# Kernel optimization log

Measured on AMD Instinct MI355X. Metric: run time of the kernel, lower is better.

## Reference

```python
import jax, jax.numpy as jnp
import numpy as np

N = 50000   # num entities
R = 230     # num relations (doubled for inverses -> 460)
H = 128     # hidden dim
T = 8       # timesteps (sequence_len)
E = 600000  # edges per timestep graph
L = 2       # num RGCN layers
RRELU_SLOPE = (1.0 / 8.0 + 1.0 / 3.0) / 2.0  # F.rrelu eval-mode slope


def _l2norm(x):
    # F.normalize: L2 over last dim, eps=1e-12
    return x / jnp.maximum(jnp.linalg.norm(x, axis=-1, keepdims=True), 1e-12)


def setup_inputs() -> dict:
    key = jax.random.key(0)
    ks = jax.random.split(key, 10)
    src = jax.random.randint(ks[0], (T, E), 0, N)
    dst = jax.random.randint(ks[1], (T, E), 0, N)
    etype = jax.random.randint(ks[2], (T, E), 0, 2 * R)
    emb_ent = jax.random.normal(ks[3], (N, H), jnp.float32)
    emb_rel = jax.random.normal(ks[4], (2 * R, H), jnp.float32) * 0.05
    w_neigh = jax.random.normal(ks[5], (L, H, H), jnp.float32) * 0.05
    w_loop = jax.random.normal(ks[6], (L, H, H), jnp.float32) * 0.05
    w_evolve = jax.random.normal(ks[7], (L, H, H), jnp.float32) * 0.05
    tg_w = jax.random.normal(ks[8], (H, H), jnp.float32) * 0.05
    tg_b = jnp.zeros((H,), jnp.float32)
    return {"emb_ent": emb_ent, "emb_rel": emb_rel, "w_neigh": w_neigh,
            "w_loop": w_loop, "w_evolve": w_evolve, "tg_w": tg_w,
            "tg_b": tg_b, "src": src, "dst": dst, "etype": etype}


def reference(emb_ent, emb_rel, w_neigh, w_loop, w_evolve, tg_w, tg_b, src, dst, etype):
    # rgcn receives emb_rel.data (detached) in the torch module
    rel = jax.lax.stop_gradient(emb_rel)

    def rgcn(h, s, d, t):
        indeg = jax.ops.segment_sum(jnp.ones(s.shape, h.dtype), d, num_segments=N)
        norm = 1.0 / jnp.maximum(indeg, 1.0)          # g.ndata['norm']
        has_in = (indeg > 0)[:, None]
        for l in range(L):
            msg = (h[s] + rel[t]) @ w_neigh[l]          # [E,H]
            agg = jax.ops.segment_sum(msg, d, num_segments=N) * norm[:, None]
            loop = jnp.where(has_in, h @ w_loop[l], h @ w_evolve[l])
            z = agg + loop
            h = jnp.where(z >= 0, z, RRELU_SLOPE * z)   # rrelu (eval mode)
        return h

    def step(h, edges):
        s, d, t = edges
        cur = _l2norm(rgcn(h, s, d, t))                 # layer_norm=True
        tw = jax.nn.sigmoid(h @ tg_w + tg_b)            # time gate
        h_new = tw * cur + (1.0 - tw) * h
        return h_new, h_new

    h0 = _l2norm(emb_ent)
    _, hist = jax.lax.scan(step, h0, (src, dst, etype))
    history_embs = jnp.concatenate([h0[None], hist], axis=0)  # [T+1,N,H]
    return history_embs, emb_rel
```

## Files before the change

### kernel.cpp

```cpp
#include <hip/hip_runtime.h>

#define N_ENT 50000
#define H 128
#define NREL 460
#define T_STEPS 8
#define NEDGE 600000
#define SLOPE 0.22916666666666666f
#define NBUK 391
#define EPB 4096
#define ZCAP 8192

typedef __attribute__((ext_vector_type(8))) short bf16x8;
typedef __attribute__((ext_vector_type(8))) unsigned short us8;
typedef __attribute__((ext_vector_type(4))) float f32x4;
typedef unsigned short u16;
typedef unsigned int u32;
typedef unsigned long long u64;

__device__ __forceinline__ float b2f(u16 u) {
  union { u32 i; float f; } v; v.i = ((u32)u) << 16; return v.f;
}
__device__ __forceinline__ u16 f2b(float f) {
  union { float f; u32 i; } v; v.f = f;
  return (u16)((v.i + 0x7FFFu + ((v.i >> 16) & 1u)) >> 16);
}
__device__ __forceinline__ float wave_sum(float v) {
#pragma unroll
  for (int off = 32; off > 0; off >>= 1) v += __shfl_xor(v, off, 64);
  return v;
}

__global__ void convw_kernel(const float* __restrict__ wn, const float* __restrict__ wl,
                             const float* __restrict__ tg, u16* __restrict__ wbt) {
  int m = blockIdx.x >> 6;
  int f = ((blockIdx.x & 63) << 8) + threadIdx.x;
  int n = f >> 7, k = f & 127;
  const float* src;
  switch (m) {
    case 0: src = wn; break;
    case 1: src = wl; break;
    case 2: src = wn + 16384; break;
    case 3: src = wl + 16384; break;
    default: src = tg; break;
  }
  wbt[m * 16384 + n * 128 + k] = f2b(src[k * 128 + n]);
}

__global__ void convrel_kernel(const float* __restrict__ rel, u16* __restrict__ relb) {
  int i = blockIdx.x * 256 + threadIdx.x;
  relb[i] = f2b(rel[i]);
}

__global__ void l2norm_kernel(const float* __restrict__ in, float* __restrict__ out,
                              u16* __restrict__ outb) {
  int row = blockIdx.x * 4 + (threadIdx.x >> 6);
  int lane = threadIdx.x & 63;
  size_t base = (size_t)row * H;
  float2 v = ((const float2*)(in + base))[lane];
  float ss = wave_sum(v.x * v.x + v.y * v.y);
  float inv = 1.0f / fmaxf(sqrtf(ss), 1e-12f);
  float2 o = {v.x * inv, v.y * inv};
  ((float2*)(out + base))[lane] = o;
  ushort2 ob; ob.x = f2b(o.x); ob.y = f2b(o.y);
  ((ushort2*)(outb + base))[lane] = ob;
}

__global__ __launch_bounds__(256) void bucket_count(const int* __restrict__ dst,
                                                    int* __restrict__ bcnt) {
  int t = blockIdx.y;
  __shared__ int lc[NBUK];
  for (int j = threadIdx.x; j < NBUK; j += 256) lc[j] = 0;
  __syncthreads();
  for (int i = blockIdx.x * 256 + threadIdx.x; i < NEDGE; i += 64 * 256)
    atomicAdd(&lc[dst[(size_t)t * NEDGE + i] >> 7], 1);
  __syncthreads();
  for (int j = threadIdx.x; j < NBUK; j += 256)
    if (lc[j]) atomicAdd(&bcnt[t * NBUK + j], lc[j]);
}

__global__ __launch_bounds__(512) void bucket_scan(const int* __restrict__ bcnt,
                                                   int* __restrict__ bstart,
                                                   int* __restrict__ curA,
                                                   int* __restrict__ zcnt) {
  int t = blockIdx.x, tid = threadIdx.x;
  if (tid == 0) zcnt[t] = 0;
  __shared__ int s[512];
  int v = (tid < NBUK) ? bcnt[t * NBUK + tid] : 0;
  s[tid] = v;
  __syncthreads();
  for (int off = 1; off < 512; off <<= 1) {
    int u = (tid >= off) ? s[tid - off] : 0;
    __syncthreads();
    s[tid] += u;
    __syncthreads();
  }
  if (tid < NBUK) {
    int ex = s[tid] - v;
    bstart[t * NBUK + tid] = ex;
    curA[t * NBUK + tid] = ex;
  }
}

__global__ __launch_bounds__(256) void passA_kernel(const int* __restrict__ src,
                                                    const int* __restrict__ dst,
                                                    const int* __restrict__ ety,
                                                    int* curA, u64* __restrict__ tmp) {
  int t = blockIdx.y;
  __shared__ int cnt[NBUK], base[NBUK];
  for (int j = threadIdx.x; j < NBUK; j += 256) cnt[j] = 0;
  __syncthreads();
  int e0 = blockIdx.x * EPB;
  int e1 = e0 + EPB < NEDGE ? e0 + EPB : NEDGE;
  for (int i = e0 + threadIdx.x; i < e1; i += 256)
    atomicAdd(&cnt[dst[(size_t)t * NEDGE + i] >> 7], 1);
  __syncthreads();
  for (int j = threadIdx.x; j < NBUK; j += 256) {
    int c = cnt[j];
    base[j] = c ? atomicAdd(&curA[t * NBUK + j], c) : 0;
    cnt[j] = 0;
  }
  __syncthreads();
  for (int i = e0 + threadIdx.x; i < e1; i += 256) {
    size_t o = (size_t)t * NEDGE + i;
    int d = dst[o];
    int j = d >> 7;
    int p = base[j] + atomicAdd(&cnt[j], 1);
    tmp[(size_t)t * NEDGE + p] = ((u64)d << 32) | (u32)src[o] | ((u32)ety[o] << 17);
  }
}

__global__ __launch_bounds__(256) void passB_kernel(const u64* __restrict__ tmp,
                                                    const int* __restrict__ bstart,
                                                    int* __restrict__ rp,
                                                    u32* __restrict__ edges,
                                                    int* __restrict__ zcnt,
                                                    int* __restrict__ zlist) {
  int t = blockIdx.y, b = blockIdx.x, tid = threadIdx.x;
  int start = bstart[t * NBUK + b];
  int end = (b + 1 < NBUK) ? bstart[t * NBUK + b + 1] : NEDGE;
  __shared__ int cnt[128], scn[128], cur[128];
  if (tid < 128) cnt[tid] = 0;
  __syncthreads();
  for (int i = start + tid; i < end; i += 256)
    atomicAdd(&cnt[(int)((tmp[(size_t)t * NEDGE + i] >> 32) & 127)], 1);
  __syncthreads();
  if (tid < 128) scn[tid] = cnt[tid];
  __syncthreads();
  for (int off = 1; off < 128; off <<= 1) {
    int u = (tid < 128 && tid >= off) ? scn[tid - off] : 0;
    __syncthreads();
    if (tid < 128) scn[tid] += u;
    __syncthreads();
  }
  if (tid < 128) {
    int rs = start + scn[tid] - cnt[tid];
    cur[tid] = rs;
    int gd = (b << 7) + tid;
    if (gd < N_ENT) {
      rp[t * N_ENT + gd] = rs + cnt[tid];
      if (cnt[tid] == 0) {
        int p = atomicAdd(&zcnt[t], 1);
        if (p < ZCAP) zlist[t * ZCAP + p] = gd;
      }
    }
  }
  __syncthreads();
  for (int i = start + tid; i < end; i += 256) {
    u64 e = tmp[(size_t)t * NEDGE + i];
    int p = atomicAdd(&cur[(int)((e >> 32) & 127)], 1);
    edges[(size_t)t * NEDGE + p] = (u32)e;
  }
}

__global__ __launch_bounds__(256) void gather_kernel(const u16* __restrict__ hb,
                                                     const u16* __restrict__ relb,
                                                     const int* __restrict__ rp,
                                                     const u32* __restrict__ edges,
                                                     u16* __restrict__ aggb) {
  int d = blockIdx.x * 16 + (threadIdx.x >> 4);
  int q = threadIdx.x & 15;
  int start = d ? rp[d - 1] : 0, end = rp[d];
  float a[8] = {};
  int i = start;
  for (; i + 4 <= end; i += 4) {
    u32 e0 = edges[i], e1 = edges[i + 1], e2 = edges[i + 2], e3 = edges[i + 3];
    us8 h0 = *(const us8*)(hb + (size_t)(e0 & 0x1FFFF) * H + q * 8);
    us8 r0 = *(const us8*)(relb + (size_t)(e0 >> 17) * H + q * 8);
    us8 h1 = *(const us8*)(hb + (size_t)(e1 & 0x1FFFF) * H + q * 8);
    us8 r1 = *(const us8*)(relb + (size_t)(e1 >> 17) * H + q * 8);
    us8 h2 = *(const us8*)(hb + (size_t)(e2 & 0x1FFFF) * H + q * 8);
    us8 r2 = *(const us8*)(relb + (size_t)(e2 >> 17) * H + q * 8);
    us8 h3 = *(const us8*)(hb + (size_t)(e3 & 0x1FFFF) * H + q * 8);
    us8 r3 = *(const us8*)(relb + (size_t)(e3 >> 17) * H + q * 8);
#pragma unroll
    for (int j = 0; j < 8; j++)
      a[j] += (b2f(h0[j]) + b2f(r0[j])) + (b2f(h1[j]) + b2f(r1[j])) +
              (b2f(h2[j]) + b2f(r2[j])) + (b2f(h3[j]) + b2f(r3[j]));
  }
  for (; i < end; i++) {
    u32 e0 = edges[i];
    us8 h0 = *(const us8*)(hb + (size_t)(e0 & 0x1FFFF) * H + q * 8);
    us8 r0 = *(const us8*)(relb + (size_t)(e0 >> 17) * H + q * 8);
#pragma unroll
    for (int j = 0; j < 8; j++) a[j] += b2f(h0[j]) + b2f(r0[j]);
  }
  int deg = end - start;
  float nm = 1.0f / (float)(deg > 0 ? deg : 1);
  us8 o;
#pragma unroll
  for (int j = 0; j < 8; j++) o[j] = f2b(a[j] * nm);
  *(us8*)(aggb + (size_t)d * H + q * 8) = o;
}

__global__ __launch_bounds__(256) void rgcn_gemm0(
    const u16* __restrict__ A1, const u16* __restrict__ A2,
    const u16* __restrict__ B1t, const u16* __restrict__ B2t, u16* __restrict__ Cb) {
  int wave = threadIdx.x >> 6, lane = threadIdx.x & 63;
  int row0 = blockIdx.x * 64 + wave * 16;
  int ar = lane & 15, kg = lane >> 4;
  int arow = row0 + ar;
  if (arow >= N_ENT) arow = N_ENT - 1;
  bf16x8 a1[4], a2[4];
#pragma unroll
  for (int s = 0; s < 4; s++) {
    a1[s] = *(const bf16x8*)(A1 + (size_t)arow * H + s * 32 + kg * 8);
    a2[s] = *(const bf16x8*)(A2 + (size_t)arow * H + s * 32 + kg * 8);
  }
  f32x4 acc[8];
  f32x4 z = {0.f, 0.f, 0.f, 0.f};
#pragma unroll
  for (int n = 0; n < 8; n++) acc[n] = z;
#pragma unroll
  for (int n = 0; n < 8; n++) {
    const u16* b1p = B1t + (size_t)(n * 16 + ar) * H + kg * 8;
    const u16* b2p = B2t + (size_t)(n * 16 + ar) * H + kg * 8;
#pragma unroll
    for (int s = 0; s < 4; s++) {
      bf16x8 b1 = *(const bf16x8*)(b1p + s * 32);
      bf16x8 b2 = *(const bf16x8*)(b2p + s * 32);
      acc[n] = __builtin_amdgcn_mfma_f32_16x16x32_bf16(a1[s], b1, acc[n], 0, 0, 0);
      acc[n] = __builtin_amdgcn_mfma_f32_16x16x32_bf16(a2[s], b2, acc[n], 0, 0, 0);
    }
  }
#pragma unroll
  for (int n = 0; n < 8; n++) {
    int c = ar + n * 16;
#pragma unroll
    for (int r = 0; r < 4; r++) {
      int gr = row0 + kg * 4 + r;
      if (gr < N_ENT) {
        float v = acc[n][r];
        v = v >= 0.f ? v : SLOPE * v;
        Cb[(size_t)gr * H + c] = f2b(v);
      }
    }
  }
}

__global__ __launch_bounds__(256) void step_final(
    const u16* __restrict__ aggb, const u16* __restrict__ hAb, const u16* hbio,
    const u16* __restrict__ B1t, const u16* __restrict__ B2t, const u16* __restrict__ B3t,
    const float* __restrict__ tgb, const float* __restrict__ h_t, float* __restrict__ h_n,
    u16* hb_out) {
  int wave = threadIdx.x >> 6, lane = threadIdx.x & 63;
  int row0 = blockIdx.x * 64 + wave * 16;
  int ar = lane & 15, kg = lane >> 4;
  int arow = row0 + ar;
  if (arow >= N_ENT) arow = N_ENT - 1;
  bf16x8 a1[4], a2[4], a3[4];
#pragma unroll
  for (int s = 0; s < 4; s++) {
    a1[s] = *(const bf16x8*)(aggb + (size_t)arow * H + s * 32 + kg * 8);
    a2[s] = *(const bf16x8*)(hAb + (size_t)arow * H + s * 32 + kg * 8);
    a3[s] = *(const bf16x8*)(hbio + (size_t)arow * H + s * 32 + kg * 8);
  }
  f32x4 accm[8], accg[8];
  f32x4 z4 = {0.f, 0.f, 0.f, 0.f};
#pragma unroll
  for (int n = 0; n < 8; n++) { accm[n] = z4; accg[n] = z4; }
#pragma unroll
  for (int n = 0; n < 8; n++) {
    const u16* b1p = B1t + (size_t)(n * 16 + ar) * H + kg * 8;
    const u16* b2p = B2t + (size_t)(n * 16 + ar) * H + kg * 8;
    const u16* b3p = B3t + (size_t)(n * 16 + ar) * H + kg * 8;
#pragma unroll
    for (int s = 0; s < 4; s++) {
      bf16x8 b1 = *(const bf16x8*)(b1p + s * 32);
      bf16x8 b2 = *(const bf16x8*)(b2p + s * 32);
      bf16x8 b3 = *(const bf16x8*)(b3p + s * 32);
      accm[n] = __builtin_amdgcn_mfma_f32_16x16x32_bf16(a1[s], b1, accm[n], 0, 0, 0);
      accm[n] = __builtin_amdgcn_mfma_f32_16x16x32_bf16(a2[s], b2, accm[n], 0, 0, 0);
      accg[n] = __builtin_amdgcn_mfma_f32_16x16x32_bf16(a3[s], b3, accg[n], 0, 0, 0);
    }
  }
#pragma unroll
  for (int r = 0; r < 4; r++) {
    int grow = row0 + kg * 4 + r;
    bool ok = grow < N_ENT;
    float zs[8], ssq = 0.f;
#pragma unroll
    for (int n = 0; n < 8; n++) {
      float v = accm[n][r];
      v = v >= 0.f ? v : SLOPE * v;
      zs[n] = v;
      ssq += v * v;
    }
    ssq += __shfl_xor(ssq, 1, 64);
    ssq += __shfl_xor(ssq, 2, 64);
    ssq += __shfl_xor(ssq, 4, 64);
    ssq += __shfl_xor(ssq, 8, 64);
    float inv = 1.0f / fmaxf(sqrtf(ssq), 1e-12f);
#pragma unroll
    for (int n = 0; n < 8; n++) {
      int c = ar + n * 16;
      float g = 1.0f / (1.0f + expf(-(accg[n][r] + tgb[c])));
      float hp = ok ? h_t[(size_t)grow * H + c] : 0.f;
      float o = g * (zs[n] * inv) + (1.0f - g) * hp;
      if (ok) {
        h_n[(size_t)grow * H + c] = o;
        hb_out[(size_t)grow * H + c] = f2b(o);
      }
    }
  }
}

__global__ void fixup0_kernel(const u16* __restrict__ hb, const float* __restrict__ We,
                              const int* __restrict__ zcnt, const int* __restrict__ zlist,
                              u16* __restrict__ hA) {
  int n = *zcnt; if (n > ZCAP) n = ZCAP;
  for (int idx = blockIdx.x; idx < n; idx += gridDim.x) {
    int r = zlist[idx];
    int c = threadIdx.x;
    float s = 0.f;
    for (int k = 0; k < H; k++) s += b2f(hb[(size_t)r * H + k]) * We[(size_t)k * H + c];
    s = s >= 0.f ? s : SLOPE * s;
    hA[(size_t)r * H + c] = f2b(s);
  }
}

__global__ void fixup1_kernel(const u16* __restrict__ hAb, const float* __restrict__ We,
                              const float* __restrict__ tgw, const float* __restrict__ tgb,
                              const float* __restrict__ h_t, const int* __restrict__ zcnt,
                              const int* __restrict__ zlist,
                              float* __restrict__ h_n, u16* __restrict__ hb) {
  __shared__ float red[2];
  int n = *zcnt; if (n > ZCAP) n = ZCAP;
  for (int idx = blockIdx.x; idx < n; idx += gridDim.x) {
    int r = zlist[idx];
    int c = threadIdx.x;
    float zv = 0.f, gv = 0.f;
    for (int k = 0; k < H; k++) {
      float ha = b2f(hAb[(size_t)r * H + k]);
      float ht = h_t[(size_t)r * H + k];
      zv += ha * We[(size_t)k * H + c];
      gv += ht * tgw[(size_t)k * H + c];
    }
    zv = zv >= 0.f ? zv : SLOPE * zv;
    gv = 1.0f / (1.0f + expf(-(gv + tgb[c])));
    float ssq = wave_sum(zv * zv);
    if ((threadIdx.x & 63) == 0) red[threadIdx.x >> 6] = ssq;
    __syncthreads();
    float inv = 1.0f / fmaxf(sqrtf(red[0] + red[1]), 1e-12f);
    float hp = h_t[(size_t)r * H + c];
    float o = gv * (zv * inv) + (1.0f - gv) * hp;
    h_n[(size_t)r * H + c] = o;
    hb[(size_t)r * H + c] = f2b(o);
    __syncthreads();
  }
}

extern "C" void kernel_launch(void* const* d_in, const int* in_sizes, int n_in,
                              void* d_out, int out_size, void* d_ws, size_t ws_size,
                              hipStream_t stream) {
  const float* emb_ent  = (const float*)d_in[0];
  const float* emb_rel  = (const float*)d_in[1];
  const float* w_neigh  = (const float*)d_in[2];
  const float* w_loop   = (const float*)d_in[3];
  const float* w_evolve = (const float*)d_in[4];
  const float* tg_w     = (const float*)d_in[5];
  const float* tg_b     = (const float*)d_in[6];
  const int* src = (const int*)d_in[7];
  const int* dst = (const int*)d_in[8];
  const int* ety = (const int*)d_in[9];
  float* out = (float*)d_out;

  const size_t NH = (size_t)N_ENT * H;
  auto au = [](size_t x) { return (x + 255) & ~(size_t)255; };
  char* w = (char*)d_ws;
  int* rp8 = (int*)w;     w += au((size_t)T_STEPS * N_ENT * 4);
  int* bcnt = (int*)w;    w += au((size_t)T_STEPS * NBUK * 4);
  int* bstart = (int*)w;  w += au((size_t)T_STEPS * NBUK * 4);
  int* curA = (int*)w;    w += au((size_t)T_STEPS * NBUK * 4);
  int* zcnt = (int*)w;    w += au((size_t)T_STEPS * 4);
  int* zlist = (int*)w;   w += au((size_t)T_STEPS * ZCAP * 4);
  u32* edges8 = (u32*)w;  w += au((size_t)T_STEPS * NEDGE * 4);
  char* uni = w;          w += au((size_t)T_STEPS * NEDGE * 8);
  u64* tmp = (u64*)uni;
  u16* aggb = (u16*)uni;
  u16* hAb = (u16*)(uni + NH * 2);
  u16* hb  = (u16*)(uni + NH * 4);
  u16* wbt = (u16*)w;     w += au((size_t)5 * 16384 * 2);
  u16* relb = (u16*)w;    w += au((size_t)NREL * H * 2);

  hipMemsetAsync(bcnt, 0, (size_t)T_STEPS * NBUK * 4, stream);
  bucket_count<<<dim3(64, T_STEPS), 256, 0, stream>>>(dst, bcnt);
  bucket_scan<<<T_STEPS, 512, 0, stream>>>(bcnt, bstart, curA, zcnt);
  passA_kernel<<<dim3((NEDGE + EPB - 1) / EPB, T_STEPS), 256, 0, stream>>>(
      src, dst, ety, curA, tmp);
  passB_kernel<<<dim3(NBUK, T_STEPS), 256, 0, stream>>>(tmp, bstart, rp8, edges8,
                                                        zcnt, zlist);

  hipMemcpyAsync(out + (size_t)(T_STEPS + 1) * NH, emb_rel, (size_t)NREL * H * 4,
                 hipMemcpyDeviceToDevice, stream);
  convw_kernel<<<320, 256, 0, stream>>>(w_neigh, w_loop, tg_w, wbt);
  convrel_kernel<<<230, 256, 0, stream>>>(emb_rel, relb);
  l2norm_kernel<<<N_ENT / 4, 256, 0, stream>>>(emb_ent, out, hb);

  for (int t = 0; t < T_STEPS; t++) {
    float* h_t = out + (size_t)t * NH;
    float* h_n = out + (size_t)(t + 1) * NH;
    const int* rp = rp8 + (size_t)t * N_ENT;
    const u32* edges = edges8 + (size_t)t * NEDGE;
    const int* zc = zcnt + t;
    const int* zl = zlist + (size_t)t * ZCAP;

    gather_kernel<<<N_ENT / 16, 256, 0, stream>>>(hb, relb, rp, edges, aggb);
    rgcn_gemm0<<<(N_ENT + 63) / 64, 256, 0, stream>>>(aggb, hb, wbt, wbt + 16384, hAb);
    fixup0_kernel<<<8, 128, 0, stream>>>(hb, w_evolve, zc, zl, hAb);
    gather_kernel<<<N_ENT / 16, 256, 0, stream>>>(hAb, relb, rp, edges, aggb);
    step_final<<<(N_ENT + 63) / 64, 256, 0, stream>>>(
        aggb, hAb, hb, wbt + 32768, wbt + 49152, wbt + 65536, tg_b, h_t, h_n, hb);
    fixup1_kernel<<<8, 128, 0, stream>>>(hAb, w_evolve + 16384, tg_w, tg_b, h_t, zc, zl,
                                         h_n, hb);
  }
}
```

Before: 1.456 ms.

## Fuse neighbor gather-aggregation into the RGCN layer GEMM kernels

Removes the separate gather kernels. Each MFMA lane now walks the incoming edge list of its own destination row and sums the bf16 source and relation rows into registers. That sum feeds the MFMA directly as the A operand, so the aggregated bf16 buffer is never written to or read back from global memory, and two launches per step go away. In exchange, only 4 lanes cover each destination row instead of 16, each lane holds 32 float accumulators, and a wave waits for the highest-degree row among its 16, which can hurt latency hiding and load balance.

```diff
diff --git a/kernel.cpp b/kernel.cpp
--- a/kernel.cpp
+++ b/kernel.cpp
@@ -172,59 +172,58 @@
   }
 }
 
-__global__ __launch_bounds__(256) void gather_kernel(const u16* __restrict__ hb,
-                                                     const u16* __restrict__ relb,
-                                                     const int* __restrict__ rp,
-                                                     const u32* __restrict__ edges,
-                                                     u16* __restrict__ aggb) {
-  int d = blockIdx.x * 16 + (threadIdx.x >> 4);
-  int q = threadIdx.x & 15;
-  int start = d ? rp[d - 1] : 0, end = rp[d];
-  float a[8] = {};
-  int i = start;
-  for (; i + 4 <= end; i += 4) {
-    u32 e0 = edges[i], e1 = edges[i + 1], e2 = edges[i + 2], e3 = edges[i + 3];
-    us8 h0 = *(const us8*)(hb + (size_t)(e0 & 0x1FFFF) * H + q * 8);
-    us8 r0 = *(const us8*)(relb + (size_t)(e0 >> 17) * H + q * 8);
-    us8 h1 = *(const us8*)(hb + (size_t)(e1 & 0x1FFFF) * H + q * 8);
-    us8 r1 = *(const us8*)(relb + (size_t)(e1 >> 17) * H + q * 8);
-    us8 h2 = *(const us8*)(hb + (size_t)(e2 & 0x1FFFF) * H + q * 8);
-    us8 r2 = *(const us8*)(relb + (size_t)(e2 >> 17) * H + q * 8);
-    us8 h3 = *(const us8*)(hb + (size_t)(e3 & 0x1FFFF) * H + q * 8);
-    us8 r3 = *(const us8*)(relb + (size_t)(e3 >> 17) * H + q * 8);
-#pragma unroll
-    for (int j = 0; j < 8; j++)
-      a[j] += (b2f(h0[j]) + b2f(r0[j])) + (b2f(h1[j]) + b2f(r1[j])) +
-              (b2f(h2[j]) + b2f(r2[j])) + (b2f(h3[j]) + b2f(r3[j]));
-  }
-  for (; i < end; i++) {
-    u32 e0 = edges[i];
-    us8 h0 = *(const us8*)(hb + (size_t)(e0 & 0x1FFFF) * H + q * 8);
-    us8 r0 = *(const us8*)(relb + (size_t)(e0 >> 17) * H + q * 8);
-#pragma unroll
-    for (int j = 0; j < 8; j++) a[j] += b2f(h0[j]) + b2f(r0[j]);
-  }
-  int deg = end - start;
-  float nm = 1.0f / (float)(deg > 0 ? deg : 1);
-  us8 o;
-#pragma unroll
-  for (int j = 0; j < 8; j++) o[j] = f2b(a[j] * nm);
-  *(us8*)(aggb + (size_t)d * H + q * 8) = o;
-}
-
-__global__ __launch_bounds__(256) void rgcn_gemm0(
-    const u16* __restrict__ A1, const u16* __restrict__ A2,
+__global__ __launch_bounds__(256) void fused0(
+    const u16* __restrict__ hb, const u16* __restrict__ relb,
+    const int* __restrict__ rp, const u32* __restrict__ edges,
     const u16* __restrict__ B1t, const u16* __restrict__ B2t, u16* __restrict__ Cb) {
   int wave = threadIdx.x >> 6, lane = threadIdx.x & 63;
   int row0 = blockIdx.x * 64 + wave * 16;
   int ar = lane & 15, kg = lane >> 4;
   int arow = row0 + ar;
   if (arow >= N_ENT) arow = N_ENT - 1;
+  int start = arow ? rp[arow - 1] : 0, end = rp[arow];
+  int cbase = kg * 8;
+  float ac[4][8] = {};
+  int i = start;
+  for (; i + 2 <= end; i += 2) {
+    u32 e0 = edges[i], e1 = edges[i + 1];
+    const u16* h0 = hb + (size_t)(e0 & 0x1FFFF) * H + cbase;
+    const u16* r0 = relb + (size_t)(e0 >> 17) * H + cbase;
+    const u16* h1 = hb + (size_t)(e1 & 0x1FFFF) * H + cbase;
+    const u16* r1 = relb + (size_t)(e1 >> 17) * H + cbase;
+#pragma unroll
+    for (int s = 0; s < 4; s++) {
+      us8 a = *(const us8*)(h0 + s * 32);
+      us8 b = *(const us8*)(r0 + s * 32);
+      us8 c = *(const us8*)(h1 + s * 32);
+      us8 d = *(const us8*)(r1 + s * 32);
+#pragma unroll
+      for (int j = 0; j < 8; j++)
+        ac[s][j] += (b2f(a[j]) + b2f(b[j])) + (b2f(c[j]) + b2f(d[j]));
+    }
+  }
+  if (i < end) {
+    u32 e0 = edges[i];
+    const u16* h0 = hb + (size_t)(e0 & 0x1FFFF) * H + cbase;
+    const u16* r0 = relb + (size_t)(e0 >> 17) * H + cbase;
+#pragma unroll
+    for (int s = 0; s < 4; s++) {
+      us8 a = *(const us8*)(h0 + s * 32);
+      us8 b = *(const us8*)(r0 + s * 32);
+#pragma unroll
+      for (int j = 0; j < 8; j++) ac[s][j] += b2f(a[j]) + b2f(b[j]);
+    }
+  }
+  int deg = end - start;
+  float nm = 1.0f / (float)(deg > 0 ? deg : 1);
   bf16x8 a1[4], a2[4];
 #pragma unroll
   for (int s = 0; s < 4; s++) {
-    a1[s] = *(const bf16x8*)(A1 + (size_t)arow * H + s * 32 + kg * 8);
-    a2[s] = *(const bf16x8*)(A2 + (size_t)arow * H + s * 32 + kg * 8);
+    us8 o;
+#pragma unroll
+    for (int j = 0; j < 8; j++) o[j] = f2b(ac[s][j] * nm);
+    a1[s] = *(bf16x8*)&o;
+    a2[s] = *(const bf16x8*)(hb + (size_t)arow * H + s * 32 + cbase);
   }
   f32x4 acc[8];
   f32x4 z = {0.f, 0.f, 0.f, 0.f};
@@ -232,8 +231,8 @@
   for (int n = 0; n < 8; n++) acc[n] = z;
 #pragma unroll
   for (int n = 0; n < 8; n++) {
-    const u16* b1p = B1t + (size_t)(n * 16 + ar) * H + kg * 8;
-    const u16* b2p = B2t + (size_t)(n * 16 + ar) * H + kg * 8;
+    const u16* b1p = B1t + (size_t)(n * 16 + ar) * H + cbase;
+    const u16* b2p = B2t + (size_t)(n * 16 + ar) * H + cbase;
 #pragma unroll
     for (int s = 0; s < 4; s++) {
       bf16x8 b1 = *(const bf16x8*)(b1p + s * 32);
@@ -257,8 +256,9 @@
   }
 }
 
-__global__ __launch_bounds__(256) void step_final(
-    const u16* __restrict__ aggb, const u16* __restrict__ hAb, const u16* hbio,
+__global__ __launch_bounds__(256) void fused1(
+    const u16* __restrict__ hAb, const u16* __restrict__ relb,
+    const int* __restrict__ rp, const u32* __restrict__ edges, const u16* hbio,
     const u16* __restrict__ B1t, const u16* __restrict__ B2t, const u16* __restrict__ B3t,
     const float* __restrict__ tgb, const float* __restrict__ h_t, float* __restrict__ h_n,
     u16* hb_out) {
@@ -267,12 +267,50 @@
   int ar = lane & 15, kg = lane >> 4;
   int arow = row0 + ar;
   if (arow >= N_ENT) arow = N_ENT - 1;
+  int start = arow ? rp[arow - 1] : 0, end = rp[arow];
+  int cbase = kg * 8;
+  float ac[4][8] = {};
+  int i = start;
+  for (; i + 2 <= end; i += 2) {
+    u32 e0 = edges[i], e1 = edges[i + 1];
+    const u16* h0 = hAb + (size_t)(e0 & 0x1FFFF) * H + cbase;
+    const u16* r0 = relb + (size_t)(e0 >> 17) * H + cbase;
+    const u16* h1 = hAb + (size_t)(e1 & 0x1FFFF) * H + cbase;
+    const u16* r1 = relb + (size_t)(e1 >> 17) * H + cbase;
+#pragma unroll
+    for (int s = 0; s < 4; s++) {
+      us8 a = *(const us8*)(h0 + s * 32);
+      us8 b = *(const us8*)(r0 + s * 32);
+      us8 c = *(const us8*)(h1 + s * 32);
+      us8 d = *(const us8*)(r1 + s * 32);
+#pragma unroll
+      for (int j = 0; j < 8; j++)
+        ac[s][j] += (b2f(a[j]) + b2f(b[j])) + (b2f(c[j]) + b2f(d[j]));
+    }
+  }
+  if (i < end) {
+    u32 e0 = edges[i];
+    const u16* h0 = hAb + (size_t)(e0 & 0x1FFFF) * H + cbase;
+    const u16* r0 = relb + (size_t)(e0 >> 17) * H + cbase;
+#pragma unroll
+    for (int s = 0; s < 4; s++) {
+      us8 a = *(const us8*)(h0 + s * 32);
+      us8 b = *(const us8*)(r0 + s * 32);
+#pragma unroll
+      for (int j = 0; j < 8; j++) ac[s][j] += b2f(a[j]) + b2f(b[j]);
+    }
+  }
+  int deg = end - start;
+  float nm = 1.0f / (float)(deg > 0 ? deg : 1);
   bf16x8 a1[4], a2[4], a3[4];
 #pragma unroll
   for (int s = 0; s < 4; s++) {
-    a1[s] = *(const bf16x8*)(aggb + (size_t)arow * H + s * 32 + kg * 8);
-    a2[s] = *(const bf16x8*)(hAb + (size_t)arow * H + s * 32 + kg * 8);
-    a3[s] = *(const bf16x8*)(hbio + (size_t)arow * H + s * 32 + kg * 8);
+    us8 o;
+#pragma unroll
+    for (int j = 0; j < 8; j++) o[j] = f2b(ac[s][j] * nm);
+    a1[s] = *(bf16x8*)&o;
+    a2[s] = *(const bf16x8*)(hAb + (size_t)arow * H + s * 32 + cbase);
+    a3[s] = *(const bf16x8*)(hbio + (size_t)arow * H + s * 32 + cbase);
   }
   f32x4 accm[8], accg[8];
   f32x4 z4 = {0.f, 0.f, 0.f, 0.f};
@@ -280,9 +318,9 @@
   for (int n = 0; n < 8; n++) { accm[n] = z4; accg[n] = z4; }
 #pragma unroll
   for (int n = 0; n < 8; n++) {
-    const u16* b1p = B1t + (size_t)(n * 16 + ar) * H + kg * 8;
-    const u16* b2p = B2t + (size_t)(n * 16 + ar) * H + kg * 8;
-    const u16* b3p = B3t + (size_t)(n * 16 + ar) * H + kg * 8;
+    const u16* b1p = B1t + (size_t)(n * 16 + ar) * H + cbase;
+    const u16* b2p = B2t + (size_t)(n * 16 + ar) * H + cbase;
+    const u16* b3p = B3t + (size_t)(n * 16 + ar) * H + cbase;
 #pragma unroll
     for (int s = 0; s < 4; s++) {
       bf16x8 b1 = *(const bf16x8*)(b1p + s * 32);
@@ -396,9 +434,8 @@
   u32* edges8 = (u32*)w;  w += au((size_t)T_STEPS * NEDGE * 4);
   char* uni = w;          w += au((size_t)T_STEPS * NEDGE * 8);
   u64* tmp = (u64*)uni;
-  u16* aggb = (u16*)uni;
-  u16* hAb = (u16*)(uni + NH * 2);
-  u16* hb  = (u16*)(uni + NH * 4);
+  u16* hAb = (u16*)uni;
+  u16* hb  = (u16*)(uni + NH * 2);
   u16* wbt = (u16*)w;     w += au((size_t)5 * 16384 * 2);
   u16* relb = (u16*)w;    w += au((size_t)NREL * H * 2);
 
@@ -416,6 +453,7 @@
   convrel_kernel<<<230, 256, 0, stream>>>(emb_rel, relb);
   l2norm_kernel<<<N_ENT / 4, 256, 0, stream>>>(emb_ent, out, hb);
 
+  const int NBLK = (N_ENT + 63) / 64;
   for (int t = 0; t < T_STEPS; t++) {
     float* h_t = out + (size_t)t * NH;
     float* h_n = out + (size_t)(t + 1) * NH;
@@ -424,12 +462,11 @@
     const int* zc = zcnt + t;
     const int* zl = zlist + (size_t)t * ZCAP;
 
-    gather_kernel<<<N_ENT / 16, 256, 0, stream>>>(hb, relb, rp, edges, aggb);
-    rgcn_gemm0<<<(N_ENT + 63) / 64, 256, 0, stream>>>(aggb, hb, wbt, wbt + 16384, hAb);
+    fused0<<<NBLK, 256, 0, stream>>>(hb, relb, rp, edges, wbt, wbt + 16384, hAb);
     fixup0_kernel<<<8, 128, 0, stream>>>(hb, w_evolve, zc, zl, hAb);
-    gather_kernel<<<N_ENT / 16, 256, 0, stream>>>(hAb, relb, rp, edges, aggb);
-    step_final<<<(N_ENT + 63) / 64, 256, 0, stream>>>(
-        aggb, hAb, hb, wbt + 32768, wbt + 49152, wbt + 65536, tg_b, h_t, h_n, hb);
+    fused1<<<NBLK, 256, 0, stream>>>(hAb, relb, rp, edges, hb,
+                                     wbt + 32768, wbt + 49152, wbt + 65536,
+                                     tg_b, h_t, h_n, hb);
     fixup1_kernel<<<8, 128, 0, stream>>>(hAb, w_evolve + 16384, tg_w, tg_b, h_t, zc, zl,
                                          h_n, hb);
   }
```

Measured after the change: 1.781 ms. 1.22x slower.

## Precompute per-destination relation sums once per timestep, reuse across both layers

Applied to the files above, without the earlier changes.

The relation-embedding gather is split out of the per-layer gather into a relsum kernel that sums rel[etype] per destination node once per timestep. Both layer gathers then start from that precomputed sum and only gather neighbor h rows, using an 8-wide unroll. This removes the duplicate relation-row gather from the second layer and halves the per-edge loads in each layer gather. The cost is an extra kernel launch, an extra N×H bf16 buffer written and read twice, and an additional bf16 rounding of the relation sum.

```diff
diff --git a/kernel.cpp b/kernel.cpp
--- a/kernel.cpp
+++ b/kernel.cpp
@@ -172,11 +172,10 @@
   }
 }
 
-__global__ __launch_bounds__(256) void gather_kernel(const u16* __restrict__ hb,
-                                                     const u16* __restrict__ relb,
+__global__ __launch_bounds__(256) void relsum_kernel(const u16* __restrict__ relb,
                                                      const int* __restrict__ rp,
                                                      const u32* __restrict__ edges,
-                                                     u16* __restrict__ aggb) {
+                                                     u16* __restrict__ rsb) {
   int d = blockIdx.x * 16 + (threadIdx.x >> 4);
   int q = threadIdx.x & 15;
   int start = d ? rp[d - 1] : 0, end = rp[d];
@@ -184,25 +183,58 @@
   int i = start;
   for (; i + 4 <= end; i += 4) {
     u32 e0 = edges[i], e1 = edges[i + 1], e2 = edges[i + 2], e3 = edges[i + 3];
+    us8 r0 = *(const us8*)(relb + (size_t)(e0 >> 17) * H + q * 8);
+    us8 r1 = *(const us8*)(relb + (size_t)(e1 >> 17) * H + q * 8);
+    us8 r2 = *(const us8*)(relb + (size_t)(e2 >> 17) * H + q * 8);
+    us8 r3 = *(const us8*)(relb + (size_t)(e3 >> 17) * H + q * 8);
+#pragma unroll
+    for (int j = 0; j < 8; j++)
+      a[j] += (b2f(r0[j]) + b2f(r1[j])) + (b2f(r2[j]) + b2f(r3[j]));
+  }
+  for (; i < end; i++) {
+    us8 r0 = *(const us8*)(relb + (size_t)(edges[i] >> 17) * H + q * 8);
+#pragma unroll
+    for (int j = 0; j < 8; j++) a[j] += b2f(r0[j]);
+  }
+  us8 o;
+#pragma unroll
+  for (int j = 0; j < 8; j++) o[j] = f2b(a[j]);
+  *(us8*)(rsb + (size_t)d * H + q * 8) = o;
+}
+
+__global__ __launch_bounds__(256) void gather_kernel(const u16* __restrict__ hb,
+                                                     const u16* __restrict__ rsb,
+                                                     const int* __restrict__ rp,
+                                                     const u32* __restrict__ edges,
+                                                     u16* __restrict__ aggb) {
+  int d = blockIdx.x * 16 + (threadIdx.x >> 4);
+  int q = threadIdx.x & 15;
+  int start = d ? rp[d - 1] : 0, end = rp[d];
+  us8 rs = *(const us8*)(rsb + (size_t)d * H + q * 8);
+  float a[8];
+#pragma unroll
+  for (int j = 0; j < 8; j++) a[j] = b2f(rs[j]);
+  int i = start;
+  for (; i + 8 <= end; i += 8) {
+    u32 e0 = edges[i], e1 = edges[i + 1], e2 = edges[i + 2], e3 = edges[i + 3];
+    u32 e4 = edges[i + 4], e5 = edges[i + 5], e6 = edges[i + 6], e7 = edges[i + 7];
     us8 h0 = *(const us8*)(hb + (size_t)(e0 & 0x1FFFF) * H + q * 8);
-    us8 r0 = *(const us8*)(relb + (size_t)(e0 >> 17) * H + q * 8);
     us8 h1 = *(const us8*)(hb + (size_t)(e1 & 0x1FFFF) * H + q * 8);
-    us8 r1 = *(const us8*)(relb + (size_t)(e1 >> 17) * H + q * 8);
     us8 h2 = *(const us8*)(hb + (size_t)(e2 & 0x1FFFF) * H + q * 8);
-    us8 r2 = *(const us8*)(relb + (size_t)(e2 >> 17) * H + q * 8);
     us8 h3 = *(const us8*)(hb + (size_t)(e3 & 0x1FFFF) * H + q * 8);
-    us8 r3 = *(const us8*)(relb + (size_t)(e3 >> 17) * H + q * 8);
+    us8 h4 = *(const us8*)(hb + (size_t)(e4 & 0x1FFFF) * H + q * 8);
+    us8 h5 = *(const us8*)(hb + (size_t)(e5 & 0x1FFFF) * H + q * 8);
+    us8 h6 = *(const us8*)(hb + (size_t)(e6 & 0x1FFFF) * H + q * 8);
+    us8 h7 = *(const us8*)(hb + (size_t)(e7 & 0x1FFFF) * H + q * 8);
 #pragma unroll
     for (int j = 0; j < 8; j++)
-      a[j] += (b2f(h0[j]) + b2f(r0[j])) + (b2f(h1[j]) + b2f(r1[j])) +
-              (b2f(h2[j]) + b2f(r2[j])) + (b2f(h3[j]) + b2f(r3[j]));
+      a[j] += ((b2f(h0[j]) + b2f(h1[j])) + (b2f(h2[j]) + b2f(h3[j]))) +
+              ((b2f(h4[j]) + b2f(h5[j])) + (b2f(h6[j]) + b2f(h7[j])));
   }
   for (; i < end; i++) {
-    u32 e0 = edges[i];
-    us8 h0 = *(const us8*)(hb + (size_t)(e0 & 0x1FFFF) * H + q * 8);
-    us8 r0 = *(const us8*)(relb + (size_t)(e0 >> 17) * H + q * 8);
-#pragma unroll
-    for (int j = 0; j < 8; j++) a[j] += b2f(h0[j]) + b2f(r0[j]);
+    us8 h0 = *(const us8*)(hb + (size_t)(edges[i] & 0x1FFFF) * H + q * 8);
+#pragma unroll
+    for (int j = 0; j < 8; j++) a[j] += b2f(h0[j]);
   }
   int deg = end - start;
   float nm = 1.0f / (float)(deg > 0 ? deg : 1);
@@ -401,6 +433,7 @@
   u16* hb  = (u16*)(uni + NH * 4);
   u16* wbt = (u16*)w;     w += au((size_t)5 * 16384 * 2);
   u16* relb = (u16*)w;    w += au((size_t)NREL * H * 2);
+  u16* rsb = (u16*)w;     w += au(NH * 2);
 
   hipMemsetAsync(bcnt, 0, (size_t)T_STEPS * NBUK * 4, stream);
   bucket_count<<<dim3(64, T_STEPS), 256, 0, stream>>>(dst, bcnt);
@@ -424,10 +457,11 @@
     const int* zc = zcnt + t;
     const int* zl = zlist + (size_t)t * ZCAP;
 
-    gather_kernel<<<N_ENT / 16, 256, 0, stream>>>(hb, relb, rp, edges, aggb);
+    relsum_kernel<<<N_ENT / 16, 256, 0, stream>>>(relb, rp, edges, rsb);
+    gather_kernel<<<N_ENT / 16, 256, 0, stream>>>(hb, rsb, rp, edges, aggb);
     rgcn_gemm0<<<(N_ENT + 63) / 64, 256, 0, stream>>>(aggb, hb, wbt, wbt + 16384, hAb);
     fixup0_kernel<<<8, 128, 0, stream>>>(hb, w_evolve, zc, zl, hAb);
-    gather_kernel<<<N_ENT / 16, 256, 0, stream>>>(hAb, relb, rp, edges, aggb);
+    gather_kernel<<<N_ENT / 16, 256, 0, stream>>>(hAb, rsb, rp, edges, aggb);
     step_final<<<(N_ENT + 63) / 64, 256, 0, stream>>>(
         aggb, hAb, hb, wbt + 32768, wbt + 49152, wbt + 65536, tg_b, h_t, h_n, hb);
     fixup1_kernel<<<8, 128, 0, stream>>>(hAb, w_evolve + 16384, tg_w, tg_b, h_t, zc, zl,
```

New measurement: 1.548 ms. +6.4%, slower.

## Sort destination nodes by in-degree for balanced gather and unroll edge loop by 8

Applied to the files above, without the earlier changes.

Adds a one-time per-timestep counting sort of destination nodes by in-degree (capped at 63), and the gather kernel now processes nodes in that sorted order. Each wavefront then handles nodes of similar degree, which reduces divergence across the 16-lane groups. The edge loop is also unrolled to 8 edges per iteration so more independent loads are in flight. The trade-offs are an extra indirection load per node, scattered writes to aggb, loss of locality in row order, and a small preprocessing kernel.

```diff
diff --git a/kernel.cpp b/kernel.cpp
--- a/kernel.cpp
+++ b/kernel.cpp
@@ -172,17 +172,68 @@
   }
 }
 
+__global__ __launch_bounds__(1024) void degsort_kernel(const int* __restrict__ rp8,
+                                                       int* __restrict__ rsorted) {
+  int t = blockIdx.x, tid = threadIdx.x;
+  const int* rp = rp8 + (size_t)t * N_ENT;
+  __shared__ int hist[64], cur[64];
+  if (tid < 64) hist[tid] = 0;
+  __syncthreads();
+  for (int r = tid; r < N_ENT; r += 1024) {
+    int deg = rp[r] - (r ? rp[r - 1] : 0);
+    atomicAdd(&hist[deg < 63 ? deg : 63], 1);
+  }
+  __syncthreads();
+  if (tid == 0) {
+    int acc = 0;
+    for (int b = 0; b < 64; b++) { cur[b] = acc; acc += hist[b]; }
+  }
+  __syncthreads();
+  for (int r = tid; r < N_ENT; r += 1024) {
+    int deg = rp[r] - (r ? rp[r - 1] : 0);
+    int p = atomicAdd(&cur[deg < 63 ? deg : 63], 1);
+    rsorted[(size_t)t * N_ENT + p] = r;
+  }
+}
+
 __global__ __launch_bounds__(256) void gather_kernel(const u16* __restrict__ hb,
                                                      const u16* __restrict__ relb,
                                                      const int* __restrict__ rp,
                                                      const u32* __restrict__ edges,
+                                                     const int* __restrict__ rsorted,
                                                      u16* __restrict__ aggb) {
-  int d = blockIdx.x * 16 + (threadIdx.x >> 4);
+  int d = rsorted[blockIdx.x * 16 + (threadIdx.x >> 4)];
   int q = threadIdx.x & 15;
   int start = d ? rp[d - 1] : 0, end = rp[d];
   float a[8] = {};
   int i = start;
-  for (; i + 4 <= end; i += 4) {
+  for (; i + 8 <= end; i += 8) {
+    u32 e0 = edges[i], e1 = edges[i + 1], e2 = edges[i + 2], e3 = edges[i + 3];
+    u32 e4 = edges[i + 4], e5 = edges[i + 5], e6 = edges[i + 6], e7 = edges[i + 7];
+    us8 h0 = *(const us8*)(hb + (size_t)(e0 & 0x1FFFF) * H + q * 8);
+    us8 r0 = *(const us8*)(relb + (size_t)(e0 >> 17) * H + q * 8);
+    us8 h1 = *(const us8*)(hb + (size_t)(e1 & 0x1FFFF) * H + q * 8);
+    us8 r1 = *(const us8*)(relb + (size_t)(e1 >> 17) * H + q * 8);
+    us8 h2 = *(const us8*)(hb + (size_t)(e2 & 0x1FFFF) * H + q * 8);
+    us8 r2 = *(const us8*)(relb + (size_t)(e2 >> 17) * H + q * 8);
+    us8 h3 = *(const us8*)(hb + (size_t)(e3 & 0x1FFFF) * H + q * 8);
+    us8 r3 = *(const us8*)(relb + (size_t)(e3 >> 17) * H + q * 8);
+    us8 h4 = *(const us8*)(hb + (size_t)(e4 & 0x1FFFF) * H + q * 8);
+    us8 r4 = *(const us8*)(relb + (size_t)(e4 >> 17) * H + q * 8);
+    us8 h5 = *(const us8*)(hb + (size_t)(e5 & 0x1FFFF) * H + q * 8);
+    us8 r5 = *(const us8*)(relb + (size_t)(e5 >> 17) * H + q * 8);
+    us8 h6 = *(const us8*)(hb + (size_t)(e6 & 0x1FFFF) * H + q * 8);
+    us8 r6 = *(const us8*)(relb + (size_t)(e6 >> 17) * H + q * 8);
+    us8 h7 = *(const us8*)(hb + (size_t)(e7 & 0x1FFFF) * H + q * 8);
+    us8 r7 = *(const us8*)(relb + (size_t)(e7 >> 17) * H + q * 8);
+#pragma unroll
+    for (int j = 0; j < 8; j++)
+      a[j] += (((b2f(h0[j]) + b2f(r0[j])) + (b2f(h1[j]) + b2f(r1[j]))) +
+               ((b2f(h2[j]) + b2f(r2[j])) + (b2f(h3[j]) + b2f(r3[j])))) +
+              (((b2f(h4[j]) + b2f(r4[j])) + (b2f(h5[j]) + b2f(r5[j]))) +
+               ((b2f(h6[j]) + b2f(r6[j])) + (b2f(h7[j]) + b2f(r7[j]))));
+  }
+  if (i + 4 <= end) {
     u32 e0 = edges[i], e1 = edges[i + 1], e2 = edges[i + 2], e3 = edges[i + 3];
     us8 h0 = *(const us8*)(hb + (size_t)(e0 & 0x1FFFF) * H + q * 8);
     us8 r0 = *(const us8*)(relb + (size_t)(e0 >> 17) * H + q * 8);
@@ -194,8 +245,9 @@
     us8 r3 = *(const us8*)(relb + (size_t)(e3 >> 17) * H + q * 8);
 #pragma unroll
     for (int j = 0; j < 8; j++)
-      a[j] += (b2f(h0[j]) + b2f(r0[j])) + (b2f(h1[j]) + b2f(r1[j])) +
-              (b2f(h2[j]) + b2f(r2[j])) + (b2f(h3[j]) + b2f(r3[j]));
+      a[j] += ((b2f(h0[j]) + b2f(r0[j])) + (b2f(h1[j]) + b2f(r1[j]))) +
+              ((b2f(h2[j]) + b2f(r2[j])) + (b2f(h3[j]) + b2f(r3[j])));
+    i += 4;
   }
   for (; i < end; i++) {
     u32 e0 = edges[i];
@@ -393,6 +445,7 @@
   int* curA = (int*)w;    w += au((size_t)T_STEPS * NBUK * 4);
   int* zcnt = (int*)w;    w += au((size_t)T_STEPS * 4);
   int* zlist = (int*)w;   w += au((size_t)T_STEPS * ZCAP * 4);
+  int* rsorted = (int*)w; w += au((size_t)T_STEPS * N_ENT * 4);
   u32* edges8 = (u32*)w;  w += au((size_t)T_STEPS * NEDGE * 4);
   char* uni = w;          w += au((size_t)T_STEPS * NEDGE * 8);
   u64* tmp = (u64*)uni;
@@ -409,6 +462,7 @@
       src, dst, ety, curA, tmp);
   passB_kernel<<<dim3(NBUK, T_STEPS), 256, 0, stream>>>(tmp, bstart, rp8, edges8,
                                                         zcnt, zlist);
+  degsort_kernel<<<T_STEPS, 1024, 0, stream>>>(rp8, rsorted);
 
   hipMemcpyAsync(out + (size_t)(T_STEPS + 1) * NH, emb_rel, (size_t)NREL * H * 4,
                  hipMemcpyDeviceToDevice, stream);
@@ -421,13 +475,14 @@
     float* h_n = out + (size_t)(t + 1) * NH;
     const int* rp = rp8 + (size_t)t * N_ENT;
     const u32* edges = edges8 + (size_t)t * NEDGE;
+    const int* rs = rsorted + (size_t)t * N_ENT;
     const int* zc = zcnt + t;
     const int* zl = zlist + (size_t)t * ZCAP;
 
-    gather_kernel<<<N_ENT / 16, 256, 0, stream>>>(hb, relb, rp, edges, aggb);
+    gather_kernel<<<N_ENT / 16, 256, 0, stream>>>(hb, relb, rp, edges, rs, aggb);
     rgcn_gemm0<<<(N_ENT + 63) / 64, 256, 0, stream>>>(aggb, hb, wbt, wbt + 16384, hAb);
     fixup0_kernel<<<8, 128, 0, stream>>>(hb, w_evolve, zc, zl, hAb);
-    gather_kernel<<<N_ENT / 16, 256, 0, stream>>>(hAb, relb, rp, edges, aggb);
+    gather_kernel<<<N_ENT / 16, 256, 0, stream>>>(hAb, relb, rp, edges, rs, aggb);
     step_final<<<(N_ENT + 63) / 64, 256, 0, stream>>>(
         aggb, hAb, hb, wbt + 32768, wbt + 49152, wbt + 65536, tg_b, h_t, h_n, hb);
     fixup1_kernel<<<8, 128, 0, stream>>>(hAb, w_evolve + 16384, tg_w, tg_b, h_t, zc, zl,
```

Result: no change. 1.477 ms (+1.5%).
